# Optimization experiments

Hardware: AMD Instinct MI355X
Metric: run time of the kernel (lower is better)

The kernel has to match this reference:

```python
import jax, jax.numpy as jnp
import numpy as np

B, L, S = 8192, 1024, 3
OUTSIDE, TM_HELIX, INSIDE = 0, 1, 2


def setup_inputs() -> dict:
    key = jax.random.key(0)
    k1, k2 = jax.random.split(key)
    emissions = jax.random.normal(k1, (B, L, S), dtype=jnp.float32)
    tags = jax.random.randint(k2, (B, L), 0, S)
    mask = jnp.ones((B, L), dtype=jnp.float32)
    t = np.zeros((S, S), dtype=np.float32)
    t[OUTSIDE, INSIDE] = -5.0
    t[INSIDE, OUTSIDE] = -5.0
    t[OUTSIDE, TM_HELIX] = 1.0
    t[INSIDE, TM_HELIX] = 1.0
    t[TM_HELIX, OUTSIDE] = 1.0
    t[TM_HELIX, INSIDE] = 1.0
    transitions = jnp.asarray(t)
    return {"emissions": emissions, "mask": mask, "transitions": transitions, "tags": tags}


def _score_sentence(emissions, tags, mask, transitions):
    # emission score of the gold tag at every position: (B, L)
    em_score = jnp.take_along_axis(emissions, tags[..., None], axis=2)[..., 0]
    # transition score between consecutive gold tags: (B, L-1)
    trans_score = transitions[tags[:, :-1], tags[:, 1:]]
    return em_score[:, 0] * mask[:, 0] + jnp.sum(
        (trans_score + em_score[:, 1:]) * mask[:, 1:], axis=1
    )


def _forward_alg(emissions, mask, transitions):
    def step(alpha, xs):
        em_t, m_t = xs  # (B, S), (B,)
        # scores[b, i, j] = alpha[b, i] + T[i, j] + em_t[b, j]
        scores = alpha[:, :, None] + transitions[None, :, :] + em_t[:, None, :]
        new_alpha = jax.nn.logsumexp(scores, axis=1)
        alpha = jnp.where(m_t[:, None] > 0, new_alpha, alpha)
        return alpha, None

    alpha0 = emissions[:, 0, :]
    xs = (jnp.swapaxes(emissions[:, 1:, :], 0, 1),  # (L-1, B, S)
          jnp.swapaxes(mask[:, 1:], 0, 1))          # (L-1, B)
    alpha, _ = jax.lax.scan(step, alpha0, xs)
    return jax.nn.logsumexp(alpha, axis=1)  # (B,)


def reference(emissions, mask, transitions, tags):
    logZ = _forward_alg(emissions, mask, transitions)
    gold = _score_sentence(emissions, tags, mask, transitions)
    return jnp.mean(logZ - gold)
```

## Files before the change

kernel.cpp:

```cpp
#include <hip/hip_runtime.h>


#define LOG2E 1.4426950408889634f
#define LN2   0.6931471805599453f

constexpr int B = 8192;
constexpr int L = 1024;
constexpr int SEQS_PER_BLOCK = 4;
constexpr int NBLK = 512;
constexpr int ITERS = B / (NBLK * SEQS_PER_BLOCK);

__device__ __forceinline__ float fexp2(float x) { return __builtin_amdgcn_exp2f(x); }
__device__ __forceinline__ float flog2(float x) { return __builtin_amdgcn_logf(x); }

__device__ __forceinline__ float f4get(const float4& v, int c) {
  return c == 0 ? v.x : (c == 1 ? v.y : (c == 2 ? v.z : v.w));
}
__device__ __forceinline__ int i4get(const int4& v, int c) {
  return c == 0 ? v.x : (c == 1 ? v.y : (c == 2 ? v.z : v.w));
}

__device__ __forceinline__ float mux3(float x0, float x1, float x2, int i) {
  return (i == 0) ? x0 : ((i == 1) ? x1 : x2);
}
__device__ __forceinline__ float trmux(const float* __restrict__ T2, int p, int c) {
  const float r0 = mux3(T2[0], T2[1], T2[2], c);
  const float r1 = mux3(T2[3], T2[4], T2[5], c);
  const float r2 = mux3(T2[6], T2[7], T2[8], c);
  return mux3(r0, r1, r2, p);
}

__device__ __forceinline__ void matmul3(float* __restrict__ D,
                                        const float* __restrict__ A,
                                        const float* __restrict__ Bm) {
  #pragma unroll
  for (int i = 0; i < 3; ++i)
    #pragma unroll
    for (int j = 0; j < 3; ++j)
      D[i * 3 + j] = A[i * 3 + 0] * Bm[0 * 3 + j] +
                     A[i * 3 + 1] * Bm[1 * 3 + j] +
                     A[i * 3 + 2] * Bm[2 * 3 + j];
}

__device__ __forceinline__ void renorm3(float* __restrict__ P, float& scale) {
  float m = P[0];
  #pragma unroll
  for (int e = 1; e < 9; ++e) m = fmaxf(m, P[e]);
  int ex;
  (void)frexpf(m, &ex);
  #pragma unroll
  for (int e = 0; e < 9; ++e) P[e] = ldexpf(P[e], -ex);
  scale += (float)ex;
}

__global__ __launch_bounds__(256, 4) void crf_main(
    const float* __restrict__ em, const float* __restrict__ mask,
    const float* __restrict__ trans, const int* __restrict__ tags,
    float* __restrict__ ws) {
  const int lane = threadIdx.x & 63;
  const int wid = threadIdx.x >> 6;
  const int gwid = blockIdx.x * SEQS_PER_BLOCK + wid;

  float T2[9], tk[9];
  #pragma unroll
  for (int e = 0; e < 9; ++e) {
    T2[e] = trans[e] * LOG2E;
    tk[e] = fexp2(T2[e]);
  }

  float wsum = 0.f;

  #pragma unroll 1
  for (int it = 0; it < ITERS; ++it) {
    const int b = it * (NBLK * SEQS_PER_BLOCK) + gwid;

    const float4* em4 = (const float4*)(em + (size_t)b * (L * 3)) + lane * 12;
    const float4* mk4 = (const float4*)(mask + (size_t)b * L) + lane * 4;
    const int4*   tg4 = (const int4*)(tags + (size_t)b * L) + lane * 4;

    float4 E[12];
    #pragma unroll
    for (int u = 0; u < 12; ++u) E[u] = em4[u];
    float4 MK[4];
    #pragma unroll
    for (int u = 0; u < 4; ++u) MK[u] = mk4[u];
    int4 TG[4];
    #pragma unroll
    for (int u = 0; u < 4; ++u) TG[u] = tg4[u];

    float P[9] = {1.f, 0.f, 0.f, 0.f, 1.f, 0.f, 0.f, 0.f, 1.f};
    float scale = 0.f, gold = 0.f;
    float a0 = 0.f, a1 = 0.f, a2 = 0.f;
    float e0_sel = 0.f, mk0 = 0.f;
    int tag0 = 0, prev = 0;

    #pragma unroll
    for (int s = 0; s < 16; ++s) {
      const float ev0 = f4get(E[(3 * s + 0) >> 2], (3 * s + 0) & 3) * LOG2E;
      const float ev1 = f4get(E[(3 * s + 1) >> 2], (3 * s + 1) & 3) * LOG2E;
      const float ev2 = f4get(E[(3 * s + 2) >> 2], (3 * s + 2) & 3) * LOG2E;
      const float m   = f4get(MK[s >> 2], s & 3);
      const int   cur = i4get(TG[s >> 2], s & 3);

      const float e = mux3(ev0, ev1, ev2, cur);
      if (s == 0) {
        e0_sel = e; mk0 = m; tag0 = cur;
      } else {
        gold = fmaf(trmux(T2, prev, cur) + e, m, gold);
      }
      prev = cur;

      const float w0 = fexp2(ev0);
      const float w1 = fexp2(ev1);
      const float w2 = fexp2(ev2);
      if (s == 0) { a0 = w0; a1 = w1; a2 = w2; }
      const bool act = (m > 0.f) && !(s == 0 && lane == 0);
      const float g  = act ? 1.f : 0.f;
      const float c1 = 1.f - g;
      const float u0 = w0 * g, u1 = w1 * g, u2 = w2 * g;
      float M[9];
      M[0] = fmaf(tk[0], u0, c1); M[1] = tk[1] * u1;           M[2] = tk[2] * u2;
      M[3] = tk[3] * u0;          M[4] = fmaf(tk[4], u1, c1);  M[5] = tk[5] * u2;
      M[6] = tk[6] * u0;          M[7] = tk[7] * u1;           M[8] = fmaf(tk[8], u2, c1);
      float N[9];
      matmul3(N, P, M);
      #pragma unroll
      for (int e2 = 0; e2 < 9; ++e2) P[e2] = N[e2];

      if (s == 7 || s == 15) renorm3(P, scale);
    }

    const int prevLast = __shfl_up(prev, 1);
    if (lane == 0) gold = fmaf(e0_sel, mk0, gold);
    else           gold = fmaf(trmux(T2, prevLast, tag0) + e0_sel, mk0, gold);
    #pragma unroll
    for (int d = 1; d < 64; d <<= 1) gold += __shfl_xor(gold, d, 64);

    #pragma unroll
    for (int d = 1; d < 64; d <<= 1) {
      float o[9];
      #pragma unroll
      for (int e = 0; e < 9; ++e) o[e] = __shfl_xor(P[e], d, 64);
      const float osc = __shfl_xor(scale, d, 64);
      const bool later = (lane & d) != 0;
      float A[9], Bm[9];
      #pragma unroll
      for (int e = 0; e < 9; ++e) {
        A[e]  = later ? o[e] : P[e];
        Bm[e] = later ? P[e] : o[e];
      }
      float N[9];
      matmul3(N, A, Bm);
      #pragma unroll
      for (int e = 0; e < 9; ++e) P[e] = N[e];
      scale += osc;
    }

    if (lane == 0) {
      const float z = a0 * (P[0] + P[1] + P[2]) +
                      a1 * (P[3] + P[4] + P[5]) +
                      a2 * (P[6] + P[7] + P[8]);
      wsum += LN2 * (scale + flog2(z) - gold);
    }
  }

  __shared__ float red[SEQS_PER_BLOCK];
  if (lane == 0) red[wid] = wsum;
  __syncthreads();
  if (threadIdx.x == 0) {
    ws[blockIdx.x] = red[0] + red[1] + red[2] + red[3];
  }
}

__global__ __launch_bounds__(256) void crf_reduce(
    const float* __restrict__ ws, float* __restrict__ out) {
  const int t = threadIdx.x;
  const float4* w4 = (const float4*)ws;
  float s = 0.f;
  if (t < 128) {
    const float4 v = w4[t];
    s = (v.x + v.y) + (v.z + v.w);
  }
  #pragma unroll
  for (int d = 1; d < 64; d <<= 1) s += __shfl_xor(s, d, 64);
  __shared__ float red[4];
  if ((t & 63) == 0) red[t >> 6] = s;
  __syncthreads();
  if (t == 0) out[0] = (red[0] + red[1] + red[2] + red[3]) * (1.0f / (float)B);
}

extern "C" void kernel_launch(void* const* d_in, const int* in_sizes, int n_in,
                              void* d_out, int out_size, void* d_ws, size_t ws_size,
                              hipStream_t stream) {
  const float* em    = (const float*)d_in[0];
  const float* mask  = (const float*)d_in[1];
  const float* trans = (const float*)d_in[2];
  const int*   tags  = (const int*)d_in[3];
  float* out = (float*)d_out;
  float* ws  = (float*)d_ws;

  crf_main<<<NBLK, 256, 0, stream>>>(em, mask, trans, tags, ws);
  crf_reduce<<<1, 256, 0, stream>>>(ws, out);
}
```

Measured before the change: 200.4 us.

## Prefetch next sequence into LDS via async global_load_lds while computing current

Each wave now stages its sequence's emissions, mask and tags into a per-wave LDS slab with direct global-to-LDS loads, then reads registers from LDS. The next sequence's loads are issued before the current sequence's compute, so memory latency overlaps the scan math. Global reads also become fully coalesced, since each lane loads consecutive 16-byte chunks instead of a strided 192-byte row. The cost is 80KB of LDS per block and launch bounds lowered from 4 to 2, which reduces occupancy. The kernel relies on manual waitcnt and sched_barrier for correctness.

```diff
diff --git a/kernel.cpp b/kernel.cpp
--- a/kernel.cpp
+++ b/kernel.cpp
@@ -9,6 +9,7 @@
 constexpr int SEQS_PER_BLOCK = 4;
 constexpr int NBLK = 512;
 constexpr int ITERS = B / (NBLK * SEQS_PER_BLOCK);
+constexpr int SLAB = 1280;
 
 __device__ __forceinline__ float fexp2(float x) { return __builtin_amdgcn_exp2f(x); }
 __device__ __forceinline__ float flog2(float x) { return __builtin_amdgcn_logf(x); }
@@ -53,7 +54,30 @@
   scale += (float)ex;
 }
 
-__global__ __launch_bounds__(256, 4) void crf_main(
+__device__ __forceinline__ void stage_seq(
+    float4* slab, const float* em, const float* mask, const int* tags,
+    int b, int lane) {
+  const float4* emG = (const float4*)em + (size_t)b * 768;
+  const float4* mkG = (const float4*)mask + (size_t)b * 256;
+  const float4* tgG = (const float4*)tags + (size_t)b * 256;
+  #pragma unroll
+  for (int u = 0; u < 12; ++u)
+    __builtin_amdgcn_global_load_lds(
+        (const __attribute__((address_space(1))) void*)(emG + 64 * u + lane),
+        (__attribute__((address_space(3))) void*)(slab + 64 * u), 16, 0, 0);
+  #pragma unroll
+  for (int u = 0; u < 4; ++u)
+    __builtin_amdgcn_global_load_lds(
+        (const __attribute__((address_space(1))) void*)(mkG + 64 * u + lane),
+        (__attribute__((address_space(3))) void*)(slab + 768 + 64 * u), 16, 0, 0);
+  #pragma unroll
+  for (int u = 0; u < 4; ++u)
+    __builtin_amdgcn_global_load_lds(
+        (const __attribute__((address_space(1))) void*)(tgG + 64 * u + lane),
+        (__attribute__((address_space(3))) void*)(slab + 1024 + 64 * u), 16, 0, 0);
+}
+
+__global__ __launch_bounds__(256, 2) void crf_main(
     const float* __restrict__ em, const float* __restrict__ mask,
     const float* __restrict__ trans, const int* __restrict__ tags,
     float* __restrict__ ws) {
@@ -61,6 +85,10 @@
   const int wid = threadIdx.x >> 6;
   const int gwid = blockIdx.x * SEQS_PER_BLOCK + wid;
 
+  __shared__ float4 sBuf[SEQS_PER_BLOCK][SLAB];
+  __shared__ float red[SEQS_PER_BLOCK];
+  float4* slab = &sBuf[wid][0];
+
   float T2[9], tk[9];
   #pragma unroll
   for (int e = 0; e < 9; ++e) {
@@ -68,25 +96,31 @@
     tk[e] = fexp2(T2[e]);
   }
 
+  stage_seq(slab, em, mask, tags, gwid, lane);
+
   float wsum = 0.f;
 
   #pragma unroll 1
   for (int it = 0; it < ITERS; ++it) {
-    const int b = it * (NBLK * SEQS_PER_BLOCK) + gwid;
-
-    const float4* em4 = (const float4*)(em + (size_t)b * (L * 3)) + lane * 12;
-    const float4* mk4 = (const float4*)(mask + (size_t)b * L) + lane * 4;
-    const int4*   tg4 = (const int4*)(tags + (size_t)b * L) + lane * 4;
+    asm volatile("s_waitcnt vmcnt(0)" ::: "memory");
 
     float4 E[12];
     #pragma unroll
-    for (int u = 0; u < 12; ++u) E[u] = em4[u];
+    for (int v = 0; v < 12; ++v) E[v] = slab[12 * lane + v];
     float4 MK[4];
     #pragma unroll
-    for (int u = 0; u < 4; ++u) MK[u] = mk4[u];
+    for (int u = 0; u < 4; ++u) MK[u] = slab[768 + 4 * lane + u];
     int4 TG[4];
     #pragma unroll
-    for (int u = 0; u < 4; ++u) TG[u] = tg4[u];
+    for (int u = 0; u < 4; ++u)
+      TG[u] = *reinterpret_cast<const int4*>(&slab[1024 + 4 * lane + u]);
+
+    asm volatile("s_waitcnt lgkmcnt(0)" ::: "memory");
+    __builtin_amdgcn_sched_barrier(0);
+
+    if (it + 1 < ITERS)
+      stage_seq(slab, em, mask, tags, (it + 1) * (NBLK * SEQS_PER_BLOCK) + gwid,
+                lane);
 
     float P[9] = {1.f, 0.f, 0.f, 0.f, 1.f, 0.f, 0.f, 0.f, 1.f};
     float scale = 0.f, gold = 0.f;
@@ -164,7 +198,6 @@
     }
   }
 
-  __shared__ float red[SEQS_PER_BLOCK];
   if (lane == 0) red[wid] = wsum;
   __syncthreads();
   if (threadIdx.x == 0) {
```

Result: no change. 201.4 us (+0.5%).
